# Kernel optimization log

Hardware: AMD Instinct MI355X
Metric: run time of the kernel (lower is better)

## Reference

```python
import jax, jax.numpy as jnp
import numpy as np

N, S, E, H = 8, 1024, 1024, 16
DK = E // H


def setup_inputs() -> dict:
    key = jax.random.key(0)
    ks = jax.random.split(key, 12)
    scale = 1.0 / np.sqrt(E)
    inp = {
        "q": jax.random.normal(ks[0], (N, S, E), jnp.float32),
        "k": jax.random.normal(ks[1], (N, S, E), jnp.float32),
        "v": jax.random.normal(ks[2], (N, S, E), jnp.float32),
        "attn_mask": jax.random.randint(ks[3], (N, S, S), 0, 2).astype(bool),
        "wq": jax.random.normal(ks[4], (E, E), jnp.float32) * scale,
        "bq": jnp.zeros((E,), jnp.float32),
        "wk": jax.random.normal(ks[5], (E, E), jnp.float32) * scale,
        "bk": jnp.zeros((E,), jnp.float32),
        "wv": jax.random.normal(ks[6], (E, E), jnp.float32) * scale,
        "bv": jnp.zeros((E,), jnp.float32),
        "wo": jax.random.normal(ks[7], (E, E), jnp.float32) * scale,
        "bo": jnp.zeros((E,), jnp.float32),
    }
    return inp


def reference(q, k, v, attn_mask, wq, bq, wk, bk, wv, bv, wo, bo):
    # Linear projections (weights stored as (E_in, E_out)), split into heads.
    qh = (q @ wq + bq).reshape(N, S, H, DK).transpose(0, 2, 1, 3)  # (N,H,S,DK)
    kh = (k @ wk + bk).reshape(N, S, H, DK).transpose(0, 2, 1, 3)
    vh = (v @ wv + bv).reshape(N, S, H, DK).transpose(0, 2, 1, 3)
    logits = jnp.einsum("nhsd,nhtd->nhst", qh, kh) / np.sqrt(DK)  # (N,H,S,S)
    eps = 1e9
    logits = jnp.where(attn_mask[:, None, :, :], -eps, logits)
    attn_weights = jax.nn.softmax(logits, axis=-1)
    # dropout layers are identity in eval mode
    o = jnp.einsum("nhst,nhtd->nhsd", attn_weights, vh)  # (N,H,S,DK)
    o = o.transpose(0, 2, 1, 3).reshape(N, S, E)
    o = o @ wo + bo
    return o, attn_weights
```

## Files before the change

kernel.cpp:

```cpp
#include <hip/hip_runtime.h>
#include <cstdint>
#include <cstddef>

#define NB 8
#define SL 1024
#define ED 1024
#define NH 16
#define DKH 64

typedef __attribute__((ext_vector_type(4))) float f32x4;
typedef __attribute__((ext_vector_type(8))) short short8;
typedef __attribute__((ext_vector_type(4))) short short4v;

__device__ __forceinline__ unsigned short bf16_rn(float x) {
    unsigned int u = __float_as_uint(x);
    u += 0x7FFFu + ((u >> 16) & 1u);
    return (unsigned short)(u >> 16);
}
__device__ __forceinline__ float bf16_f(unsigned short h) {
    return __uint_as_float(((unsigned int)h) << 16);
}
__device__ __forceinline__ void split2(float x, unsigned short& hi, unsigned short& lo) {
    unsigned short h = bf16_rn(x);
    hi = h;
    lo = bf16_rn(x - bf16_f(h));
}

__device__ __forceinline__ void dma16(const unsigned short* src, unsigned short* dst) {
    __builtin_amdgcn_global_load_lds(
        (const __attribute__((address_space(1))) void*)src,
        (__attribute__((address_space(3))) void*)dst,
        16, 0, 0);
}

template<int ROWS>
__device__ __forceinline__ void dma_plane(
    const unsigned short* __restrict__ g, unsigned short* l,
    int ld, int r0, int k0, int wave, int lane)
{
    for (int i = wave; i < ROWS / 16; i += 4) {
        const unsigned short* src =
            g + (size_t)(r0 + i * 16 + (lane >> 2)) * ld + k0 + (lane & 3) * 8;
        dma16(src, l + i * 512);
    }
}

template<bool APRE, int BM, int BN, int WR, int WC, int ROWG, int COLT>
__device__ __forceinline__ void gemm_core3(
    unsigned short* smem,
    const float* __restrict__ Af,
    const unsigned short* __restrict__ Ahg, const unsigned short* __restrict__ Alg,
    int lda,
    const unsigned short* __restrict__ Bhg, const unsigned short* __restrict__ Blg,
    int ldb, int Kd, int m0, int n0,
    f32x4 (&acc)[ROWG][COLT])
{
    static_assert(WR * WC == 4, "4 waves");
    static_assert(16 * ROWG * WR == BM, "rows");
    static_assert(16 * COLT * WC == BN, "cols");
    static_assert(APRE || BM == 128, "fp32 staging assumes BM=128");

    constexpr int ASZ = BM * 32;
    constexpr int BSZ = BN * 32;
    unsigned short* Ah = smem;
    unsigned short* Al = smem + 2 * ASZ;
    unsigned short* Bh = smem + 4 * ASZ;
    unsigned short* Bl = smem + 4 * ASZ + 2 * BSZ;

    const int tid  = threadIdx.x;
    const int wave = tid >> 6;
    const int lane = tid & 63;
    const int quad = lane >> 4;
    const int l16  = lane & 15;
    const int wr   = wave / WC;
    const int wc   = wave % WC;

#pragma unroll
    for (int g = 0; g < ROWG; g++)
#pragma unroll
        for (int jt = 0; jt < COLT; jt++) acc[g][jt] = (f32x4)(0.0f);

    const int ar  = tid >> 1;
    const int acb = (tid & 1) * 2;

    auto load_a = [&](int kk, float4 st[4]) {
        const float* p = Af + (size_t)(m0 + ar) * lda + kk + (tid & 1) * 16;
        st[0] = *(const float4*)(p + 0);
        st[1] = *(const float4*)(p + 4);
        st[2] = *(const float4*)(p + 8);
        st[3] = *(const float4*)(p + 12);
    };
    auto write_a = [&](int b, const float4 st[4]) {
        unsigned short* dh = Ah + b * ASZ;
        unsigned short* dl = Al + b * ASZ;
#pragma unroll
        for (int w = 0; w < 2; w++) {
            const int csw = (acb + w) ^ ((ar >> 1) & 3);
            const float4 u0 = st[2 * w], u1 = st[2 * w + 1];
            short8 h8, l8;
            unsigned short h, l;
            split2(u0.x, h, l); h8[0] = (short)h; l8[0] = (short)l;
            split2(u0.y, h, l); h8[1] = (short)h; l8[1] = (short)l;
            split2(u0.z, h, l); h8[2] = (short)h; l8[2] = (short)l;
            split2(u0.w, h, l); h8[3] = (short)h; l8[3] = (short)l;
            split2(u1.x, h, l); h8[4] = (short)h; l8[4] = (short)l;
            split2(u1.y, h, l); h8[5] = (short)h; l8[5] = (short)l;
            split2(u1.z, h, l); h8[6] = (short)h; l8[6] = (short)l;
            split2(u1.w, h, l); h8[7] = (short)h; l8[7] = (short)l;
            *(short8*)&dh[ar * 32 + csw * 8] = h8;
            *(short8*)&dl[ar * 32 + csw * 8] = l8;
        }
    };
    auto stage_b = [&](int b, int kk) {
        dma_plane<BN>(Bhg, Bh + b * BSZ, ldb, n0, kk, wave, lane);
        dma_plane<BN>(Blg, Bl + b * BSZ, ldb, n0, kk, wave, lane);
    };
    auto stage_a_dma = [&](int b, int kk) {
        dma_plane<BM>(Ahg, Ah + b * ASZ, lda, m0, kk, wave, lane);
        dma_plane<BM>(Alg, Al + b * ASZ, lda, m0, kk, wave, lane);
    };

    if constexpr (APRE) {
        stage_a_dma(0, 0);
    } else {
        float4 st[4];
        load_a(0, st);
        write_a(0, st);
    }
    stage_b(0, 0);
    __syncthreads();

    int buf = 0;
    for (int k0 = 0; k0 < Kd; k0 += 32) {
        const int nk = k0 + 32;
        float4 st[4];
        if (nk < Kd) {
            if constexpr (APRE) stage_a_dma(buf ^ 1, nk);
            else                load_a(nk, st);
            stage_b(buf ^ 1, nk);
        }
        const unsigned short* pAh = Ah + buf * ASZ;
        const unsigned short* pAl = Al + buf * ASZ;
        const unsigned short* pBh = Bh + buf * BSZ;
        const unsigned short* pBl = Bl + buf * BSZ;
        short8 ah[ROWG], al[ROWG];
#pragma unroll
        for (int g = 0; g < ROWG; g++) {
            const int row = wr * (16 * ROWG) + g * 16 + l16;
            int co;
            if constexpr (APRE) co = quad * 8;
            else                co = (quad ^ ((row >> 1) & 3)) * 8;
            ah[g] = *(const short8*)&pAh[row * 32 + co];
            al[g] = *(const short8*)&pAl[row * 32 + co];
        }
#pragma unroll
        for (int jt = 0; jt < COLT; jt++) {
            const int brow = wc * (16 * COLT) + jt * 16 + l16;
            const short8 bh = *(const short8*)&pBh[brow * 32 + quad * 8];
            const short8 bl = *(const short8*)&pBl[brow * 32 + quad * 8];
#pragma unroll
            for (int g = 0; g < ROWG; g++) {
                acc[g][jt] = __builtin_amdgcn_mfma_f32_16x16x32_bf16(al[g], bh, acc[g][jt], 0, 0, 0);
                acc[g][jt] = __builtin_amdgcn_mfma_f32_16x16x32_bf16(ah[g], bl, acc[g][jt], 0, 0, 0);
                acc[g][jt] = __builtin_amdgcn_mfma_f32_16x16x32_bf16(ah[g], bh, acc[g][jt], 0, 0, 0);
            }
        }
        if constexpr (!APRE) {
            if (nk < Kd) write_a(buf ^ 1, st);
        }
        __syncthreads();
        buf ^= 1;
    }
}

__global__ __launch_bounds__(256)
void k_wsplitT(const float* __restrict__ W,
               unsigned short* __restrict__ Th, unsigned short* __restrict__ Tl)
{
    __shared__ float tile[64 * 65];
    const int n0 = blockIdx.x * 64;
    const int k0 = blockIdx.y * 64;
    const int tid = threadIdx.x;
    for (int i = tid; i < 64 * 64; i += 256) {
        const int rk = i >> 6, cn = i & 63;
        tile[rk * 65 + cn] = W[(size_t)(k0 + rk) * ED + n0 + cn];
    }
    __syncthreads();
    for (int i = tid; i < 64 * 64; i += 256) {
        const int rn = i >> 6, ck = i & 63;
        unsigned short h, l;
        split2(tile[ck * 65 + rn], h, l);
        Th[(size_t)(n0 + rn) * ED + k0 + ck] = h;
        Tl[(size_t)(n0 + rn) * ED + k0 + ck] = l;
    }
}

__global__ __launch_bounds__(256)
void k_projQK(const float* __restrict__ X,
              const unsigned short* __restrict__ Wh, const unsigned short* __restrict__ Wl,
              const float* __restrict__ bias,
              unsigned short* __restrict__ Oh, unsigned short* __restrict__ Ol)
{
    __shared__ unsigned short smem[(128 + 128) * 128];
    const int m0 = blockIdx.x * 128;
    const int n0 = blockIdx.y * 128;
    f32x4 acc[4][4];
    gemm_core3<false, 128, 128, 2, 2, 4, 4>(smem, X, nullptr, nullptr, ED,
                                            Wh, Wl, ED, ED, m0, n0, acc);

    const int tid = threadIdx.x, wave = tid >> 6, lane = tid & 63;
    const int quad = lane >> 4, l16 = lane & 15;
    const int wr = wave >> 1, wc = wave & 1;
#pragma unroll
    for (int jt = 0; jt < 4; jt++) {
        const int col = n0 + wc * 64 + jt * 16 + l16;
        const int h = col >> 6, d = col & 63;
        const float b = bias[col];
#pragma unroll
        for (int g = 0; g < 4; g++) {
#pragma unroll
            for (int rr = 0; rr < 4; rr++) {
                const int m = m0 + wr * 64 + g * 16 + quad * 4 + rr;
                const int n = m >> 10, s = m & 1023;
                const size_t idx = (((size_t)(n * NH + h)) * SL + s) * DKH + d;
                unsigned short hh, ll;
                split2(acc[g][jt][rr] + b, hh, ll);
                Oh[idx] = hh;
                Ol[idx] = ll;
            }
        }
    }
}

__global__ __launch_bounds__(256)
void k_projV(const float* __restrict__ X,
             const unsigned short* __restrict__ Wh, const unsigned short* __restrict__ Wl,
             const float* __restrict__ bias,
             unsigned short* __restrict__ Th, unsigned short* __restrict__ Tl)
{
    __shared__ unsigned short smem[(128 + 64) * 128];
    const int m0 = blockIdx.x * 128;
    const int n0 = blockIdx.y * 64;
    f32x4 acc[2][4];
    gemm_core3<false, 128, 64, 4, 1, 2, 4>(smem, X, nullptr, nullptr, ED,
                                           Wh, Wl, ED, ED, m0, n0, acc);

    unsigned int* T = (unsigned int*)smem;
    const int tid = threadIdx.x, wave = tid >> 6, lane = tid & 63;
    const int quad = lane >> 4, l16 = lane & 15;
#pragma unroll
    for (int jt = 0; jt < 4; jt++) {
        const int d = jt * 16 + l16;
        const float b = bias[n0 + d];
#pragma unroll
        for (int g = 0; g < 2; g++) {
#pragma unroll
            for (int rr = 0; rr < 4; rr++) {
                const int sl = wave * 32 + g * 16 + quad * 4 + rr;
                unsigned short hh, ll;
                split2(acc[g][jt][rr] + b, hh, ll);
                T[sl * 65 + d] = (unsigned int)hh | ((unsigned int)ll << 16);
            }
        }
    }
    __syncthreads();
    const int d  = tid >> 2;
    const int sc = (tid & 3) * 32;
    const int ghead = (m0 >> 10) * NH + (n0 >> 6);
    const size_t rowbase = ((size_t)ghead * DKH + d) * SL + (m0 & 1023) + sc;
#pragma unroll
    for (int c = 0; c < 4; c++) {
        short8 h8, l8;
#pragma unroll
        for (int i = 0; i < 8; i++) {
            const unsigned int u = T[(sc + c * 8 + i) * 65 + d];
            h8[i] = (short)(u & 0xFFFFu);
            l8[i] = (short)(u >> 16);
        }
        *(short8*)(Th + rowbase + c * 8) = h8;
        *(short8*)(Tl + rowbase + c * 8) = l8;
    }
}

#define PFW 68
__global__ __launch_bounds__(512)
void k_attn_fused(const unsigned short* __restrict__ qh_h, const unsigned short* __restrict__ qh_l,
                  const unsigned short* __restrict__ kh_h, const unsigned short* __restrict__ kh_l,
                  const unsigned short* __restrict__ vT_h, const unsigned short* __restrict__ vT_l,
                  const int* __restrict__ mask, float* __restrict__ attn,
                  unsigned short* __restrict__ Oh, unsigned short* __restrict__ Ol)
{
    __shared__ float Pf[8][16][PFW];
    __shared__ float MX[4][32];
    __shared__ float SMm[4][32];

    const int head = blockIdx.y;
    const int n = head >> 4, h = head & 15;
    const int m0 = blockIdx.x * 32;
    const int tid = threadIdx.x, wave = tid >> 6, lane = tid & 63;
    const int quad = lane >> 4, l16 = lane & 15;
    const int rg = wave >> 2, cq = wave & 3;

    const size_t hb = (size_t)head * SL * DKH;

    short8 qa_h[2], qa_l[2];
    {
        const unsigned short* qrh = qh_h + hb + (size_t)(m0 + rg * 16 + l16) * DKH + quad * 8;
        const unsigned short* qrl = qh_l + hb + (size_t)(m0 + rg * 16 + l16) * DKH + quad * 8;
#pragma unroll
        for (int kc = 0; kc < 2; kc++) {
            qa_h[kc] = *(const short8*)(qrh + kc * 32);
            qa_l[kc] = *(const short8*)(qrl + kc * 32);
        }
    }

    f32x4 acc[16];
    {
        const unsigned short* kbh = kh_h + hb + (size_t)(cq * 256 + l16) * DKH + quad * 8;
        const unsigned short* kbl = kh_l + hb + (size_t)(cq * 256 + l16) * DKH + quad * 8;
#pragma unroll
        for (int tt = 0; tt < 16; tt++) {
            const size_t toff = (size_t)tt * 16 * DKH;
            const short8 bh0 = *(const short8*)(kbh + toff);
            const short8 bl0 = *(const short8*)(kbl + toff);
            const short8 bh1 = *(const short8*)(kbh + toff + 32);
            const short8 bl1 = *(const short8*)(kbl + toff + 32);
            f32x4 a = (f32x4)(0.0f);
            a = __builtin_amdgcn_mfma_f32_16x16x32_bf16(qa_l[0], bh0, a, 0, 0, 0);
            a = __builtin_amdgcn_mfma_f32_16x16x32_bf16(qa_h[0], bl0, a, 0, 0, 0);
            a = __builtin_amdgcn_mfma_f32_16x16x32_bf16(qa_h[0], bh0, a, 0, 0, 0);
            a = __builtin_amdgcn_mfma_f32_16x16x32_bf16(qa_l[1], bh1, a, 0, 0, 0);
            a = __builtin_amdgcn_mfma_f32_16x16x32_bf16(qa_h[1], bl1, a, 0, 0, 0);
            a = __builtin_amdgcn_mfma_f32_16x16x32_bf16(qa_h[1], bh1, a, 0, 0, 0);
            acc[tt] = a;
        }
    }

    const int* mrow0 = mask + ((size_t)n * SL + (m0 + rg * 16 + quad * 4 + 0)) * SL + cq * 256 + l16;
    const int* mrow1 = mrow0 + SL;
    const int* mrow2 = mrow1 + SL;
    const int* mrow3 = mrow2 + SL;
#pragma unroll
    for (int tt = 0; tt < 16; tt++) {
        const int t = tt * 16;
        float v0 = acc[tt][0] * 0.125f; if (mrow0[t]) v0 = -1e9f; acc[tt][0] = v0;
        float v1 = acc[tt][1] * 0.125f; if (mrow1[t]) v1 = -1e9f; acc[tt][1] = v1;
        float v2 = acc[tt][2] * 0.125f; if (mrow2[t]) v2 = -1e9f; acc[tt][2] = v2;
        float v3 = acc[tt][3] * 0.125f; if (mrow3[t]) v3 = -1e9f; acc[tt][3] = v3;
    }

    float m4[4];
#pragma unroll
    for (int rr = 0; rr < 4; rr++) {
        float mx = -3.4e38f;
#pragma unroll
        for (int tt = 0; tt < 16; tt++) mx = fmaxf(mx, acc[tt][rr]);
#pragma unroll
        for (int o = 8; o > 0; o >>= 1) mx = fmaxf(mx, __shfl_xor(mx, o));
        m4[rr] = mx;
    }
    if (l16 < 4) {
        const float v = (l16 == 0) ? m4[0] : (l16 == 1) ? m4[1] : (l16 == 2) ? m4[2] : m4[3];
        MX[cq][rg * 16 + quad * 4 + l16] = v;
    }
    __syncthreads();
    float mc[4], sum4[4];
#pragma unroll
    for (int rr = 0; rr < 4; rr++) {
        const int r = rg * 16 + quad * 4 + rr;
        mc[rr] = fmaxf(fmaxf(MX[0][r], MX[1][r]), fmaxf(MX[2][r], MX[3][r]));
        sum4[rr] = 0.0f;
    }

#pragma unroll
    for (int tt = 0; tt < 16; tt++) {
#pragma unroll
        for (int rr = 0; rr < 4; rr++) {
            const float p = __expf(acc[tt][rr] - mc[rr]);
            acc[tt][rr] = p;
            sum4[rr] += p;
        }
    }
#pragma unroll
    for (int rr = 0; rr < 4; rr++) {
#pragma unroll
        for (int o = 8; o > 0; o >>= 1) sum4[rr] += __shfl_xor(sum4[rr], o);
    }
    if (l16 < 4) {
        const float v = (l16 == 0) ? sum4[0] : (l16 == 1) ? sum4[1] : (l16 == 2) ? sum4[2] : sum4[3];
        SMm[cq][rg * 16 + quad * 4 + l16] = v;
    }
    __syncthreads();
    float inv[4];
#pragma unroll
    for (int rr = 0; rr < 4; rr++) {
        const int r = rg * 16 + quad * 4 + rr;
        inv[rr] = 1.0f / (SMm[0][r] + SMm[1][r] + SMm[2][r] + SMm[3][r]);
    }

    f32x4 oac[4];
#pragma unroll
    for (int nt = 0; nt < 4; nt++) oac[nt] = (f32x4)(0.0f);

    const unsigned short* vbh = vT_h + (size_t)head * DKH * SL + (size_t)l16 * SL + cq * 256 + quad * 8;
    const unsigned short* vbl = vT_l + (size_t)head * DKH * SL + (size_t)l16 * SL + cq * 256 + quad * 8;
    float* aw = attn + ((size_t)head * SL + (m0 + rg * 16)) * SL + cq * 256;
    const int srow = lane >> 2;
    const int sseg = (lane & 3) * 16;

#pragma unroll
    for (int c = 0; c < 4; c++) {
#pragma unroll
        for (int i = 0; i < 4; i++) {
            const int tt = c * 4 + i;
            Pf[wave][quad * 4 + 0][i * 16 + l16] = acc[tt][0] * inv[0];
            Pf[wave][quad * 4 + 1][i * 16 + l16] = acc[tt][1] * inv[1];
            Pf[wave][quad * 4 + 2][i * 16 + l16] = acc[tt][2] * inv[2];
            Pf[wave][quad * 4 + 3][i * 16 + l16] = acc[tt][3] * inv[3];
        }
        {
            float* dst = aw + (size_t)srow * SL + c * 64 + sseg;
            const float* srcb = &Pf[wave][srow][sseg];
            const f32x4 w0 = *(const f32x4*)(srcb + 0);
            const f32x4 w1 = *(const f32x4*)(srcb + 4);
            const f32x4 w2 = *(const f32x4*)(srcb + 8);
            const f32x4 w3 = *(const f32x4*)(srcb + 12);
            *(f32x4*)(dst + 0)  = w0;
            *(f32x4*)(dst + 4)  = w1;
            *(f32x4*)(dst + 8)  = w2;
            *(f32x4*)(dst + 12) = w3;
        }
#pragma unroll
        for (int ks = 0; ks < 2; ks++) {
            const float* pr = &Pf[wave][l16][ks * 32 + quad * 8];
            const f32x4 p0 = *(const f32x4*)(pr + 0);
            const f32x4 p1 = *(const f32x4*)(pr + 4);
            short8 ph, pl;
            {
                unsigned short hh, ll;
                split2(p0[0], hh, ll); ph[0] = (short)hh; pl[0] = (short)ll;
                split2(p0[1], hh, ll); ph[1] = (short)hh; pl[1] = (short)ll;
                split2(p0[2], hh, ll); ph[2] = (short)hh; pl[2] = (short)ll;
                split2(p0[3], hh, ll); ph[3] = (short)hh; pl[3] = (short)ll;
                split2(p1[0], hh, ll); ph[4] = (short)hh; pl[4] = (short)ll;
                split2(p1[1], hh, ll); ph[5] = (short)hh; pl[5] = (short)ll;
                split2(p1[2], hh, ll); ph[6] = (short)hh; pl[6] = (short)ll;
                split2(p1[3], hh, ll); ph[7] = (short)hh; pl[7] = (short)ll;
            }
            const size_t koff = (size_t)(c * 64 + ks * 32);
#pragma unroll
            for (int nt = 0; nt < 4; nt++) {
                const short8 bh = *(const short8*)(vbh + (size_t)nt * 16 * SL + koff);
                const short8 bl = *(const short8*)(vbl + (size_t)nt * 16 * SL + koff);
                oac[nt] = __builtin_amdgcn_mfma_f32_16x16x32_bf16(pl, bh, oac[nt], 0, 0, 0);
                oac[nt] = __builtin_amdgcn_mfma_f32_16x16x32_bf16(ph, bl, oac[nt], 0, 0, 0);
                oac[nt] = __builtin_amdgcn_mfma_f32_16x16x32_bf16(ph, bh, oac[nt], 0, 0, 0);
            }
        }
    }

    __syncthreads();
#pragma unroll
    for (int nt = 0; nt < 4; nt++) {
        Pf[wave][quad * 4 + 0][nt * 16 + l16] = oac[nt][0];
        Pf[wave][quad * 4 + 1][nt * 16 + l16] = oac[nt][1];
        Pf[wave][quad * 4 + 2][nt * 16 + l16] = oac[nt][2];
        Pf[wave][quad * 4 + 3][nt * 16 + l16] = oac[nt][3];
    }
    __syncthreads();
    {
        const int r  = tid >> 4;
        const int dc = (tid & 15) * 4;
        const int rgc = r >> 4, rl = r & 15;
        short4v h4, l4;
#pragma unroll
        for (int i = 0; i < 4; i++) {
            const float v = Pf[rgc * 4 + 0][rl][dc + i] + Pf[rgc * 4 + 1][rl][dc + i]
                          + Pf[rgc * 4 + 2][rl][dc + i] + Pf[rgc * 4 + 3][rl][dc + i];
            unsigned short hh, ll;
            split2(v, hh, ll);
            h4[i] = (short)hh;
            l4[i] = (short)ll;
        }
        const size_t oidx = ((size_t)n * SL + (m0 + r)) * ED + h * DKH + dc;
        *(short4v*)(Oh + oidx) = h4;
        *(short4v*)(Ol + oidx) = l4;
    }
}

__global__ __launch_bounds__(256)
void k_outproj(const unsigned short* __restrict__ Ah, const unsigned short* __restrict__ Al,
               const unsigned short* __restrict__ Wh, const unsigned short* __restrict__ Wl,
               const float* __restrict__ bias, float* __restrict__ out)
{
    __shared__ unsigned short smem[(128 + 128) * 128];
    const int m0 = blockIdx.x * 128;
    const int n0 = blockIdx.y * 128;
    f32x4 acc[4][4];
    gemm_core3<true, 128, 128, 2, 2, 4, 4>(smem, nullptr, Ah, Al, ED,
                                           Wh, Wl, ED, ED, m0, n0, acc);

    const int tid = threadIdx.x, wave = tid >> 6, lane = tid & 63;
    const int quad = lane >> 4, l16 = lane & 15;
    const int wr = wave >> 1, wc = wave & 1;
#pragma unroll
    for (int jt = 0; jt < 4; jt++) {
        const int col = n0 + wc * 64 + jt * 16 + l16;
        const float b = bias[col];
#pragma unroll
        for (int g = 0; g < 4; g++) {
#pragma unroll
            for (int rr = 0; rr < 4; rr++) {
                const int m = m0 + wr * 64 + g * 16 + quad * 4 + rr;
                out[(size_t)m * ED + col] = acc[g][jt][rr] + b;
            }
        }
    }
}

extern "C" void kernel_launch(void* const* d_in, const int* in_sizes, int n_in,
                              void* d_out, int out_size, void* d_ws, size_t ws_size,
                              hipStream_t stream) {
    const float* q    = (const float*)d_in[0];
    const float* k    = (const float*)d_in[1];
    const float* v    = (const float*)d_in[2];
    const int*   mask = (const int*)d_in[3];
    const float* wq = (const float*)d_in[4];
    const float* bq = (const float*)d_in[5];
    const float* wk = (const float*)d_in[6];
    const float* bk = (const float*)d_in[7];
    const float* wv = (const float*)d_in[8];
    const float* bv = (const float*)d_in[9];
    const float* wo = (const float*)d_in[10];
    const float* bo = (const float*)d_in[11];

    float* out  = (float*)d_out;
    float* attn = out + (size_t)NB * SL * ED;

    unsigned short* w = (unsigned short*)d_ws;
    const size_t WPL = (size_t)ED * ED;
    unsigned short* wqT_h = w + 0 * WPL;
    unsigned short* wqT_l = w + 1 * WPL;
    unsigned short* wkT_h = w + 2 * WPL;
    unsigned short* wkT_l = w + 3 * WPL;
    unsigned short* wvT_h = w + 4 * WPL;
    unsigned short* wvT_l = w + 5 * WPL;
    unsigned short* woT_h = w + 6 * WPL;
    unsigned short* woT_l = w + 7 * WPL;
    unsigned short* base  = w + 8 * WPL;
    const size_t HPL = (size_t)NB * NH * SL * DKH;
    unsigned short* qh_h = base + 0 * HPL;
    unsigned short* qh_l = base + 1 * HPL;
    unsigned short* kh_h = base + 2 * HPL;
    unsigned short* kh_l = base + 3 * HPL;
    unsigned short* vT_h = base + 4 * HPL;
    unsigned short* vT_l = base + 5 * HPL;
    unsigned short* oh_h = qh_h;
    unsigned short* oh_l = qh_l;

    const dim3 blk(256);
    const dim3 gw(ED / 64, ED / 64);
    hipLaunchKernelGGL(k_wsplitT, gw, blk, 0, stream, wq, wqT_h, wqT_l);
    hipLaunchKernelGGL(k_wsplitT, gw, blk, 0, stream, wk, wkT_h, wkT_l);
    hipLaunchKernelGGL(k_wsplitT, gw, blk, 0, stream, wv, wvT_h, wvT_l);
    hipLaunchKernelGGL(k_wsplitT, gw, blk, 0, stream, wo, woT_h, woT_l);

    const dim3 gproj(8192 / 128, ED / 128);
    hipLaunchKernelGGL(k_projQK, gproj, blk, 0, stream, q, wqT_h, wqT_l, bq, qh_h, qh_l);
    hipLaunchKernelGGL(k_projQK, gproj, blk, 0, stream, k, wkT_h, wkT_l, bk, kh_h, kh_l);

    const dim3 gprojV(8192 / 128, ED / 64);
    hipLaunchKernelGGL(k_projV, gprojV, blk, 0, stream, v, wvT_h, wvT_l, bv, vT_h, vT_l);

    const dim3 gfa(SL / 32, NB * NH);
    hipLaunchKernelGGL(k_attn_fused, gfa, dim3(512), 0, stream,
                       qh_h, qh_l, kh_h, kh_l, vT_h, vT_l, mask, attn, oh_h, oh_l);

    hipLaunchKernelGGL(k_outproj, gproj, blk, 0, stream, oh_h, oh_l, woT_h, woT_l, bo, out);
}
```

Measured before the change: 1.561 ms.

## Presplit inputs to bf16, bitpack mask, retile V and shrink attention blocks

```diff
diff --git a/kernel.cpp b/kernel.cpp
--- a/kernel.cpp
+++ b/kernel.cpp
@@ -45,10 +45,9 @@
     }
 }
 
-template<bool APRE, int BM, int BN, int WR, int WC, int ROWG, int COLT>
-__device__ __forceinline__ void gemm_core3(
+template<int BM, int BN, int WR, int WC, int ROWG, int COLT>
+__device__ __forceinline__ void gemm_core4(
     unsigned short* smem,
-    const float* __restrict__ Af,
     const unsigned short* __restrict__ Ahg, const unsigned short* __restrict__ Alg,
     int lda,
     const unsigned short* __restrict__ Bhg, const unsigned short* __restrict__ Blg,
@@ -58,7 +57,6 @@
     static_assert(WR * WC == 4, "4 waves");
     static_assert(16 * ROWG * WR == BM, "rows");
     static_assert(16 * COLT * WC == BN, "cols");
-    static_assert(APRE || BM == 128, "fp32 staging assumes BM=128");
 
     constexpr int ASZ = BM * 32;
     constexpr int BSZ = BN * 32;
@@ -80,65 +78,20 @@
 #pragma unroll
         for (int jt = 0; jt < COLT; jt++) acc[g][jt] = (f32x4)(0.0f);
 
-    const int ar  = tid >> 1;
-    const int acb = (tid & 1) * 2;
-
-    auto load_a = [&](int kk, float4 st[4]) {
-        const float* p = Af + (size_t)(m0 + ar) * lda + kk + (tid & 1) * 16;
-        st[0] = *(const float4*)(p + 0);
-        st[1] = *(const float4*)(p + 4);
-        st[2] = *(const float4*)(p + 8);
-        st[3] = *(const float4*)(p + 12);
-    };
-    auto write_a = [&](int b, const float4 st[4]) {
-        unsigned short* dh = Ah + b * ASZ;
-        unsigned short* dl = Al + b * ASZ;
-#pragma unroll
-        for (int w = 0; w < 2; w++) {
-            const int csw = (acb + w) ^ ((ar >> 1) & 3);
-            const float4 u0 = st[2 * w], u1 = st[2 * w + 1];
-            short8 h8, l8;
-            unsigned short h, l;
-            split2(u0.x, h, l); h8[0] = (short)h; l8[0] = (short)l;
-            split2(u0.y, h, l); h8[1] = (short)h; l8[1] = (short)l;
-            split2(u0.z, h, l); h8[2] = (short)h; l8[2] = (short)l;
-            split2(u0.w, h, l); h8[3] = (short)h; l8[3] = (short)l;
-            split2(u1.x, h, l); h8[4] = (short)h; l8[4] = (short)l;
-            split2(u1.y, h, l); h8[5] = (short)h; l8[5] = (short)l;
-            split2(u1.z, h, l); h8[6] = (short)h; l8[6] = (short)l;
-            split2(u1.w, h, l); h8[7] = (short)h; l8[7] = (short)l;
-            *(short8*)&dh[ar * 32 + csw * 8] = h8;
-            *(short8*)&dl[ar * 32 + csw * 8] = l8;
-        }
-    };
-    auto stage_b = [&](int b, int kk) {
+    auto stage = [&](int b, int kk) {
+        dma_plane<BM>(Ahg, Ah + b * ASZ, lda, m0, kk, wave, lane);
+        dma_plane<BM>(Alg, Al + b * ASZ, lda, m0, kk, wave, lane);
         dma_plane<BN>(Bhg, Bh + b * BSZ, ldb, n0, kk, wave, lane);
         dma_plane<BN>(Blg, Bl + b * BSZ, ldb, n0, kk, wave, lane);
     };
-    auto stage_a_dma = [&](int b, int kk) {
-        dma_plane<BM>(Ahg, Ah + b * ASZ, lda, m0, kk, wave, lane);
-        dma_plane<BM>(Alg, Al + b * ASZ, lda, m0, kk, wave, lane);
-    };
-
-    if constexpr (APRE) {
-        stage_a_dma(0, 0);
-    } else {
-        float4 st[4];
-        load_a(0, st);
-        write_a(0, st);
-    }
-    stage_b(0, 0);
+
+    stage(0, 0);
     __syncthreads();
 
     int buf = 0;
     for (int k0 = 0; k0 < Kd; k0 += 32) {
         const int nk = k0 + 32;
-        float4 st[4];
-        if (nk < Kd) {
-            if constexpr (APRE) stage_a_dma(buf ^ 1, nk);
-            else                load_a(nk, st);
-            stage_b(buf ^ 1, nk);
-        }
+        if (nk < Kd) stage(buf ^ 1, nk);
         const unsigned short* pAh = Ah + buf * ASZ;
         const unsigned short* pAl = Al + buf * ASZ;
         const unsigned short* pBh = Bh + buf * BSZ;
@@ -147,11 +100,8 @@
 #pragma unroll
         for (int g = 0; g < ROWG; g++) {
             const int row = wr * (16 * ROWG) + g * 16 + l16;
-            int co;
-            if constexpr (APRE) co = quad * 8;
-            else                co = (quad ^ ((row >> 1) & 3)) * 8;
-            ah[g] = *(const short8*)&pAh[row * 32 + co];
-            al[g] = *(const short8*)&pAl[row * 32 + co];
+            ah[g] = *(const short8*)&pAh[row * 32 + quad * 8];
+            al[g] = *(const short8*)&pAl[row * 32 + quad * 8];
         }
 #pragma unroll
         for (int jt = 0; jt < COLT; jt++) {
@@ -164,9 +114,6 @@
                 acc[g][jt] = __builtin_amdgcn_mfma_f32_16x16x32_bf16(ah[g], bl, acc[g][jt], 0, 0, 0);
                 acc[g][jt] = __builtin_amdgcn_mfma_f32_16x16x32_bf16(ah[g], bh, acc[g][jt], 0, 0, 0);
             }
-        }
-        if constexpr (!APRE) {
-            if (nk < Kd) write_a(buf ^ 1, st);
         }
         __syncthreads();
         buf ^= 1;
@@ -196,7 +143,45 @@
 }
 
 __global__ __launch_bounds__(256)
-void k_projQK(const float* __restrict__ X,
+void k_splitX(const float* __restrict__ X,
+              unsigned short* __restrict__ Xh, unsigned short* __restrict__ Xl)
+{
+    const size_t i = ((size_t)blockIdx.x * 256 + threadIdx.x) * 8;
+    const float4 v0 = *(const float4*)(X + i);
+    const float4 v1 = *(const float4*)(X + i + 4);
+    short8 h8, l8;
+    unsigned short h, l;
+    split2(v0.x, h, l); h8[0] = (short)h; l8[0] = (short)l;
+    split2(v0.y, h, l); h8[1] = (short)h; l8[1] = (short)l;
+    split2(v0.z, h, l); h8[2] = (short)h; l8[2] = (short)l;
+    split2(v0.w, h, l); h8[3] = (short)h; l8[3] = (short)l;
+    split2(v1.x, h, l); h8[4] = (short)h; l8[4] = (short)l;
+    split2(v1.y, h, l); h8[5] = (short)h; l8[5] = (short)l;
+    split2(v1.z, h, l); h8[6] = (short)h; l8[6] = (short)l;
+    split2(v1.w, h, l); h8[7] = (short)h; l8[7] = (short)l;
+    *(short8*)(Xh + i) = h8;
+    *(short8*)(Xl + i) = l8;
+}
+
+__global__ __launch_bounds__(256)
+void k_maskpack(const int* __restrict__ m, unsigned int* __restrict__ mb)
+{
+    const size_t w = (size_t)blockIdx.x * 256 + threadIdx.x;
+    const int4* p = (const int4*)(m + w * 32);
+    unsigned int b = 0;
+#pragma unroll
+    for (int i = 0; i < 8; i++) {
+        const int4 q4 = p[i];
+        b |= (q4.x ? 1u : 0u) << (i * 4 + 0);
+        b |= (q4.y ? 1u : 0u) << (i * 4 + 1);
+        b |= (q4.z ? 1u : 0u) << (i * 4 + 2);
+        b |= (q4.w ? 1u : 0u) << (i * 4 + 3);
+    }
+    mb[w] = b;
+}
+
+__global__ __launch_bounds__(256)
+void k_projQK(const unsigned short* __restrict__ Xh, const unsigned short* __restrict__ Xl,
               const unsigned short* __restrict__ Wh, const unsigned short* __restrict__ Wl,
               const float* __restrict__ bias,
               unsigned short* __restrict__ Oh, unsigned short* __restrict__ Ol)
@@ -205,8 +190,7 @@
     const int m0 = blockIdx.x * 128;
     const int n0 = blockIdx.y * 128;
     f32x4 acc[4][4];
-    gemm_core3<false, 128, 128, 2, 2, 4, 4>(smem, X, nullptr, nullptr, ED,
-                                            Wh, Wl, ED, ED, m0, n0, acc);
+    gemm_core4<128, 128, 2, 2, 4, 4>(smem, Xh, Xl, ED, Wh, Wl, ED, ED, m0, n0, acc);
 
     const int tid = threadIdx.x, wave = tid >> 6, lane = tid & 63;
     const int quad = lane >> 4, l16 = lane & 15;
@@ -233,7 +217,7 @@
 }
 
 __global__ __launch_bounds__(256)
-void k_projV(const float* __restrict__ X,
+void k_projV(const unsigned short* __restrict__ Xh, const unsigned short* __restrict__ Xl,
              const unsigned short* __restrict__ Wh, const unsigned short* __restrict__ Wl,
              const float* __restrict__ bias,
              unsigned short* __restrict__ Th, unsigned short* __restrict__ Tl)
@@ -242,8 +226,7 @@
     const int m0 = blockIdx.x * 128;
     const int n0 = blockIdx.y * 64;
     f32x4 acc[2][4];
-    gemm_core3<false, 128, 64, 4, 1, 2, 4>(smem, X, nullptr, nullptr, ED,
-                                           Wh, Wl, ED, ED, m0, n0, acc);
+    gemm_core4<128, 64, 4, 1, 2, 4>(smem, Xh, Xl, ED, Wh, Wl, ED, ED, m0, n0, acc);
 
     unsigned int* T = (unsigned int*)smem;
     const int tid = threadIdx.x, wave = tid >> 6, lane = tid & 63;
@@ -267,7 +250,8 @@
     const int d  = tid >> 2;
     const int sc = (tid & 3) * 32;
     const int ghead = (m0 >> 10) * NH + (n0 >> 6);
-    const size_t rowbase = ((size_t)ghead * DKH + d) * SL + (m0 & 1023) + sc;
+    const int sblk = ((m0 & 1023) + sc) >> 5;
+    const size_t base = (size_t)ghead * (SL * DKH) + ((size_t)sblk * DKH + d) * 32;
 #pragma unroll
     for (int c = 0; c < 4; c++) {
         short8 h8, l8;
@@ -277,41 +261,38 @@
             h8[i] = (short)(u & 0xFFFFu);
             l8[i] = (short)(u >> 16);
         }
-        *(short8*)(Th + rowbase + c * 8) = h8;
-        *(short8*)(Tl + rowbase + c * 8) = l8;
+        *(short8*)(Th + base + c * 8) = h8;
+        *(short8*)(Tl + base + c * 8) = l8;
     }
 }
 
 #define PFW 68
-__global__ __launch_bounds__(512)
+__global__ __launch_bounds__(256, 4)
 void k_attn_fused(const unsigned short* __restrict__ qh_h, const unsigned short* __restrict__ qh_l,
                   const unsigned short* __restrict__ kh_h, const unsigned short* __restrict__ kh_l,
-                  const unsigned short* __restrict__ vT_h, const unsigned short* __restrict__ vT_l,
-                  const int* __restrict__ mask, float* __restrict__ attn,
+                  const unsigned short* __restrict__ v3_h, const unsigned short* __restrict__ v3_l,
+                  const unsigned int* __restrict__ maskb, float* __restrict__ attn,
                   unsigned short* __restrict__ Oh, unsigned short* __restrict__ Ol)
 {
-    __shared__ float Pf[8][16][PFW];
-    __shared__ float MX[4][32];
-    __shared__ float SMm[4][32];
+    __shared__ float Pf[4][16][PFW];
+    __shared__ float MX[4][16];
+    __shared__ float SMm[4][16];
 
     const int head = blockIdx.y;
     const int n = head >> 4, h = head & 15;
-    const int m0 = blockIdx.x * 32;
-    const int tid = threadIdx.x, wave = tid >> 6, lane = tid & 63;
+    const int m0 = blockIdx.x * 16;
+    const int tid = threadIdx.x, cq = tid >> 6, lane = tid & 63;
     const int quad = lane >> 4, l16 = lane & 15;
-    const int rg = wave >> 2, cq = wave & 3;
-
     const size_t hb = (size_t)head * SL * DKH;
 
     short8 qa_h[2], qa_l[2];
     {
-        const unsigned short* qrh = qh_h + hb + (size_t)(m0 + rg * 16 + l16) * DKH + quad * 8;
-        const unsigned short* qrl = qh_l + hb + (size_t)(m0 + rg * 16 + l16) * DKH + quad * 8;
-#pragma unroll
-        for (int kc = 0; kc < 2; kc++) {
-            qa_h[kc] = *(const short8*)(qrh + kc * 32);
-            qa_l[kc] = *(const short8*)(qrl + kc * 32);
-        }
+        const unsigned short* qrh = qh_h + hb + (size_t)(m0 + l16) * DKH + quad * 8;
+        const unsigned short* qrl = qh_l + hb + (size_t)(m0 + l16) * DKH + quad * 8;
+        qa_h[0] = *(const short8*)(qrh);
+        qa_l[0] = *(const short8*)(qrl);
+        qa_h[1] = *(const short8*)(qrh + 32);
+        qa_l[1] = *(const short8*)(qrl + 32);
     }
 
     f32x4 acc[16];
@@ -336,17 +317,22 @@
         }
     }
 
-    const int* mrow0 = mask + ((size_t)n * SL + (m0 + rg * 16 + quad * 4 + 0)) * SL + cq * 256 + l16;
-    const int* mrow1 = mrow0 + SL;
-    const int* mrow2 = mrow1 + SL;
-    const int* mrow3 = mrow2 + SL;
-#pragma unroll
-    for (int tt = 0; tt < 16; tt++) {
-        const int t = tt * 16;
-        float v0 = acc[tt][0] * 0.125f; if (mrow0[t]) v0 = -1e9f; acc[tt][0] = v0;
-        float v1 = acc[tt][1] * 0.125f; if (mrow1[t]) v1 = -1e9f; acc[tt][1] = v1;
-        float v2 = acc[tt][2] * 0.125f; if (mrow2[t]) v2 = -1e9f; acc[tt][2] = v2;
-        float v3 = acc[tt][3] * 0.125f; if (mrow3[t]) v3 = -1e9f; acc[tt][3] = v3;
+    {
+        const unsigned int* mw = maskb + ((size_t)n * SL + (m0 + quad * 4)) * (SL / 32) + cq * 8;
+        const unsigned int bmlo = 1u << l16;
+        const unsigned int bmhi = 1u << (16 + l16);
+#pragma unroll
+        for (int rr = 0; rr < 4; rr++) {
+            const uint4 wa = *(const uint4*)(mw + (size_t)rr * (SL / 32));
+            const uint4 wb = *(const uint4*)(mw + (size_t)rr * (SL / 32) + 4);
+            const unsigned int wd[8] = {wa.x, wa.y, wa.z, wa.w, wb.x, wb.y, wb.z, wb.w};
+#pragma unroll
+            for (int tt = 0; tt < 16; tt++) {
+                float v = acc[tt][rr] * 0.125f;
+                if (wd[tt >> 1] & ((tt & 1) ? bmhi : bmlo)) v = -1e9f;
+                acc[tt][rr] = v;
+            }
+        }
     }
 
     float m4[4];
@@ -361,13 +347,13 @@
     }
     if (l16 < 4) {
         const float v = (l16 == 0) ? m4[0] : (l16 == 1) ? m4[1] : (l16 == 2) ? m4[2] : m4[3];
-        MX[cq][rg * 16 + quad * 4 + l16] = v;
+        MX[cq][quad * 4 + l16] = v;
     }
     __syncthreads();
     float mc[4], sum4[4];
 #pragma unroll
     for (int rr = 0; rr < 4; rr++) {
-        const int r = rg * 16 + quad * 4 + rr;
+        const int r = quad * 4 + rr;
         mc[rr] = fmaxf(fmaxf(MX[0][r], MX[1][r]), fmaxf(MX[2][r], MX[3][r]));
         sum4[rr] = 0.0f;
     }
@@ -388,13 +374,13 @@
     }
     if (l16 < 4) {
         const float v = (l16 == 0) ? sum4[0] : (l16 == 1) ? sum4[1] : (l16 == 2) ? sum4[2] : sum4[3];
-        SMm[cq][rg * 16 + quad * 4 + l16] = v;
+        SMm[cq][quad * 4 + l16] = v;
     }
     __syncthreads();
     float inv[4];
 #pragma unroll
     for (int rr = 0; rr < 4; rr++) {
-        const int r = rg * 16 + quad * 4 + rr;
+        const int r = quad * 4 + rr;
         inv[rr] = 1.0f / (SMm[0][r] + SMm[1][r] + SMm[2][r] + SMm[3][r]);
     }
 
@@ -402,9 +388,9 @@
 #pragma unroll
     for (int nt = 0; nt < 4; nt++) oac[nt] = (f32x4)(0.0f);
 
-    const unsigned short* vbh = vT_h + (size_t)head * DKH * SL + (size_t)l16 * SL + cq * 256 + quad * 8;
-    const unsigned short* vbl = vT_l + (size_t)head * DKH * SL + (size_t)l16 * SL + cq * 256 + quad * 8;
-    float* aw = attn + ((size_t)head * SL + (m0 + rg * 16)) * SL + cq * 256;
+    const unsigned short* v3bh = v3_h + (size_t)head * (SL * DKH);
+    const unsigned short* v3bl = v3_l + (size_t)head * (SL * DKH);
+    float* aw = attn + ((size_t)head * SL + m0) * SL + cq * 256;
     const int srow = lane >> 2;
     const int sseg = (lane & 3) * 16;
 
@@ -413,26 +399,22 @@
 #pragma unroll
         for (int i = 0; i < 4; i++) {
             const int tt = c * 4 + i;
-            Pf[wave][quad * 4 + 0][i * 16 + l16] = acc[tt][0] * inv[0];
-            Pf[wave][quad * 4 + 1][i * 16 + l16] = acc[tt][1] * inv[1];
-            Pf[wave][quad * 4 + 2][i * 16 + l16] = acc[tt][2] * inv[2];
-            Pf[wave][quad * 4 + 3][i * 16 + l16] = acc[tt][3] * inv[3];
+            Pf[cq][quad * 4 + 0][i * 16 + l16] = acc[tt][0] * inv[0];
+            Pf[cq][quad * 4 + 1][i * 16 + l16] = acc[tt][1] * inv[1];
+            Pf[cq][quad * 4 + 2][i * 16 + l16] = acc[tt][2] * inv[2];
+            Pf[cq][quad * 4 + 3][i * 16 + l16] = acc[tt][3] * inv[3];
         }
         {
             float* dst = aw + (size_t)srow * SL + c * 64 + sseg;
-            const float* srcb = &Pf[wave][srow][sseg];
-            const f32x4 w0 = *(const f32x4*)(srcb + 0);
-            const f32x4 w1 = *(const f32x4*)(srcb + 4);
-            const f32x4 w2 = *(const f32x4*)(srcb + 8);
-            const f32x4 w3 = *(const f32x4*)(srcb + 12);
-            *(f32x4*)(dst + 0)  = w0;
-            *(f32x4*)(dst + 4)  = w1;
-            *(f32x4*)(dst + 8)  = w2;
-            *(f32x4*)(dst + 12) = w3;
+            const float* srcb = &Pf[cq][srow][sseg];
+            __builtin_nontemporal_store(*(const f32x4*)(srcb + 0),  (f32x4*)(dst + 0));
+            __builtin_nontemporal_store(*(const f32x4*)(srcb + 4),  (f32x4*)(dst + 4));
+            __builtin_nontemporal_store(*(const f32x4*)(srcb + 8),  (f32x4*)(dst + 8));
+            __builtin_nontemporal_store(*(const f32x4*)(srcb + 12), (f32x4*)(dst + 12));
         }
 #pragma unroll
         for (int ks = 0; ks < 2; ks++) {
-            const float* pr = &Pf[wave][l16][ks * 32 + quad * 8];
+            const float* pr = &Pf[cq][l16][ks * 32 + quad * 8];
             const f32x4 p0 = *(const f32x4*)(pr + 0);
             const f32x4 p1 = *(const f32x4*)(pr + 4);
             short8 ph, pl;
@@ -447,11 +429,12 @@
                 split2(p1[2], hh, ll); ph[6] = (short)hh; pl[6] = (short)ll;
                 split2(p1[3], hh, ll); ph[7] = (short)hh; pl[7] = (short)ll;
             }
-            const size_t koff = (size_t)(c * 64 + ks * 32);
+            const int tc = cq * 8 + c * 2 + ks;
 #pragma unroll
             for (int nt = 0; nt < 4; nt++) {
-                const short8 bh = *(const short8*)(vbh + (size_t)nt * 16 * SL + koff);
-                const short8 bl = *(const short8*)(vbl + (size_t)nt * 16 * SL + koff);
+                const size_t vo = ((size_t)(tc * 64 + nt * 16 + l16)) * 32 + quad * 8;
+                const short8 bh = *(const short8*)(v3bh + vo);
+                const short8 bl = *(const short8*)(v3bl + vo);
                 oac[nt] = __builtin_amdgcn_mfma_f32_16x16x32_bf16(pl, bh, oac[nt], 0, 0, 0);
                 oac[nt] = __builtin_amdgcn_mfma_f32_16x16x32_bf16(ph, bl, oac[nt], 0, 0, 0);
                 oac[nt] = __builtin_amdgcn_mfma_f32_16x16x32_bf16(ph, bh, oac[nt], 0, 0, 0);
@@ -462,27 +445,26 @@
     __syncthreads();
 #pragma unroll
     for (int nt = 0; nt < 4; nt++) {
-        Pf[wave][quad * 4 + 0][nt * 16 + l16] = oac[nt][0];
-        Pf[wave][quad * 4 + 1][nt * 16 + l16] = oac[nt][1];
-        Pf[wave][quad * 4 + 2][nt * 16 + l16] = oac[nt][2];
-        Pf[wave][quad * 4 + 3][nt * 16 + l16] = oac[nt][3];
+        Pf[cq][quad * 4 + 0][nt * 16 + l16] = oac[nt][0];
+        Pf[cq][quad * 4 + 1][nt * 16 + l16] = oac[nt][1];
+        Pf[cq][quad * 4 + 2][nt * 16 + l16] = oac[nt][2];
+        Pf[cq][quad * 4 + 3][nt * 16 + l16] = oac[nt][3];
     }
     __syncthreads();
     {
         const int r  = tid >> 4;
         const int dc = (tid & 15) * 4;
-        const int rgc = r >> 4, rl = r & 15;
         short4v h4, l4;
 #pragma unroll
         for (int i = 0; i < 4; i++) {
-            const float v = Pf[rgc * 4 + 0][rl][dc + i] + Pf[rgc * 4 + 1][rl][dc + i]
-                          + Pf[rgc * 4 + 2][rl][dc + i] + Pf[rgc * 4 + 3][rl][dc + i];
+            const float v = Pf[0][r][dc + i] + Pf[1][r][dc + i]
+                          + Pf[2][r][dc + i] + Pf[3][r][dc + i];
             unsigned short hh, ll;
             split2(v, hh, ll);
             h4[i] = (short)hh;
             l4[i] = (short)ll;
         }
-        const size_t oidx = ((size_t)n * SL + (m0 + r)) * ED + h * DKH + dc;
+        const size_t oidx = ((size_t)n * SL + m0 + r) * ED + h * DKH + dc;
         *(short4v*)(Oh + oidx) = h4;
         *(short4v*)(Ol + oidx) = l4;
     }
@@ -497,8 +479,7 @@
     const int m0 = blockIdx.x * 128;
     const int n0 = blockIdx.y * 128;
     f32x4 acc[4][4];
-    gemm_core3<true, 128, 128, 2, 2, 4, 4>(smem, nullptr, Ah, Al, ED,
-                                           Wh, Wl, ED, ED, m0, n0, acc);
+    gemm_core4<128, 128, 2, 2, 4, 4>(smem, Ah, Al, ED, Wh, Wl, ED, ED, m0, n0, acc);
 
     const int tid = threadIdx.x, wave = tid >> 6, lane = tid & 63;
     const int quad = lane >> 4, l16 = lane & 15;
@@ -536,6 +517,16 @@
 
     float* out  = (float*)d_out;
     float* attn = out + (size_t)NB * SL * ED;
+    const size_t attnElems = (size_t)NB * NH * SL * SL;
+
+    const size_t HPL = (size_t)NB * NH * SL * DKH;
+    unsigned short* xs = (unsigned short*)(attn + attnElems) - 6 * HPL;
+    unsigned short* xq_h = xs + 0 * HPL;
+    unsigned short* xq_l = xs + 1 * HPL;
+    unsigned short* xk_h = xs + 2 * HPL;
+    unsigned short* xk_l = xs + 3 * HPL;
+    unsigned short* xv_h = xs + 4 * HPL;
+    unsigned short* xv_l = xs + 5 * HPL;
 
     unsigned short* w = (unsigned short*)d_ws;
     const size_t WPL = (size_t)ED * ED;
@@ -548,33 +539,50 @@
     unsigned short* woT_h = w + 6 * WPL;
     unsigned short* woT_l = w + 7 * WPL;
     unsigned short* base  = w + 8 * WPL;
-    const size_t HPL = (size_t)NB * NH * SL * DKH;
     unsigned short* qh_h = base + 0 * HPL;
     unsigned short* qh_l = base + 1 * HPL;
     unsigned short* kh_h = base + 2 * HPL;
     unsigned short* kh_l = base + 3 * HPL;
-    unsigned short* vT_h = base + 4 * HPL;
-    unsigned short* vT_l = base + 5 * HPL;
-    unsigned short* oh_h = qh_h;
-    unsigned short* oh_l = qh_l;
+    unsigned short* v3_h = base + 4 * HPL;
+    unsigned short* v3_l = base + 5 * HPL;
+    unsigned int*  maskb = (unsigned int*)(base + 6 * HPL);
+    unsigned short* afterMb = base + 6 * HPL + (NB * SL * SL / 32) * 2;
+
+    const size_t needBytes = (size_t)(afterMb - w) * 2 + 2 * HPL * 2;
+    unsigned short* oh_h;
+    unsigned short* oh_l;
+    if (ws_size >= needBytes) {
+        oh_h = afterMb;
+        oh_l = afterMb + HPL;
+    } else {
+        oh_h = qh_h;
+        oh_l = qh_l;
+    }
 
     const dim3 blk(256);
+
+    const dim3 gsx((NB * SL * ED) / (8 * 256));
+    hipLaunchKernelGGL(k_splitX, gsx, blk, 0, stream, q, xq_h, xq_l);
+    hipLaunchKernelGGL(k_splitX, gsx, blk, 0, stream, k, xk_h, xk_l);
+    hipLaunchKernelGGL(k_splitX, gsx, blk, 0, stream, v, xv_h, xv_l);
+
     const dim3 gw(ED / 64, ED / 64);
     hipLaunchKernelGGL(k_wsplitT, gw, blk, 0, stream, wq, wqT_h, wqT_l);
     hipLaunchKernelGGL(k_wsplitT, gw, blk, 0, stream, wk, wkT_h, wkT_l);
     hipLaunchKernelGGL(k_wsplitT, gw, blk, 0, stream, wv, wvT_h, wvT_l);
     hipLaunchKernelGGL(k_wsplitT, gw, blk, 0, stream, wo, woT_h, woT_l);
 
+    hipLaunchKernelGGL(k_maskpack, dim3((NB * SL * SL / 32) / 256), blk, 0, stream, mask, maskb);
+
     const dim3 gproj(8192 / 128, ED / 128);
-    hipLaunchKernelGGL(k_projQK, gproj, blk, 0, stream, q, wqT_h, wqT_l, bq, qh_h, qh_l);
-    hipLaunchKernelGGL(k_projQK, gproj, blk, 0, stream, k, wkT_h, wkT_l, bk, kh_h, kh_l);
-
+    hipLaunchKernelGGL(k_projQK, gproj, blk, 0, stream, xq_h, xq_l, wqT_h, wqT_l, bq, qh_h, qh_l);
+    hipLaunchKernelGGL(k_projQK, gproj, blk, 0, stream, xk_h, xk_l, wkT_h, wkT_l, bk, kh_h, kh_l);
     const dim3 gprojV(8192 / 128, ED / 64);
-    hipLaunchKernelGGL(k_projV, gprojV, blk, 0, stream, v, wvT_h, wvT_l, bv, vT_h, vT_l);
-
-    const dim3 gfa(SL / 32, NB * NH);
-    hipLaunchKernelGGL(k_attn_fused, gfa, dim3(512), 0, stream,
-                       qh_h, qh_l, kh_h, kh_l, vT_h, vT_l, mask, attn, oh_h, oh_l);
+    hipLaunchKernelGGL(k_projV, gprojV, blk, 0, stream, xv_h, xv_l, wvT_h, wvT_l, bv, v3_h, v3_l);
+
+    const dim3 gfa(SL / 16, NB * NH);
+    hipLaunchKernelGGL(k_attn_fused, gfa, blk, 0, stream,
+                       qh_h, qh_l, kh_h, kh_l, v3_h, v3_l, maskb, attn, oh_h, oh_l);
 
     hipLaunchKernelGGL(k_outproj, gproj, blk, 0, stream, oh_h, oh_l, woT_h, woT_l, bo, out);
 }
```

Result: faster. 1.445 ms (-7.5%).
